# Performance work log

Hardware: AMD Instinct MI355X
Metric: run time of the kernel (lower is better)

Reference implementation:

```python
import jax, jax.numpy as jnp
import numpy as np

DIM = 2048
HID = 2730  # dim*mlp_ratio // (1 + top_k)
E = 8
K = 2
B, T = 4, 2048


def setup_inputs() -> dict:
    key = jax.random.key(0)
    ks = jax.random.split(key, 8)
    s = 0.02
    return {
        "x": jax.random.normal(ks[0], (B, T, DIM), jnp.float32),
        "router_w": jax.random.normal(ks[1], (DIM, E), jnp.float32) * s,
        "sw1": jax.random.normal(ks[2], (DIM, HID), jnp.float32) * s,
        "sw2": jax.random.normal(ks[3], (HID, DIM), jnp.float32) * s,
        "sw3": jax.random.normal(ks[4], (DIM, HID), jnp.float32) * s,
        "ew1": jax.random.normal(ks[5], (E, DIM, HID), jnp.float32) * s,
        "ew2": jax.random.normal(ks[6], (E, HID, DIM), jnp.float32) * s,
        "ew3": jax.random.normal(ks[7], (E, DIM, HID), jnp.float32) * s,
    }


def _expert(x, w1, w2, w3):
    return (jax.nn.silu(x @ w1) * (x @ w3)) @ w2


def reference(x, router_w, sw1, sw2, sw3, ew1, ew2, ew3):
    # eval-mode forward (no router noise, no aux loss)
    out = _expert(x, sw1, sw2, sw3)  # shared expert, [B,T,C]
    logits = x @ router_w            # [B,T,E]
    probs = jax.nn.softmax(logits, axis=-1)
    topv, topi = jax.lax.top_k(probs, K)           # [B,T,K]
    topv = topv / topv.sum(-1, keepdims=True)      # renormalize
    # dense combine weights [B,T,E]: w[...,e] = sum_k topv_k * (topi_k == e)
    onehot = jax.nn.one_hot(topi, E, dtype=x.dtype)  # [B,T,K,E]
    w = jnp.einsum("btk,btke->bte", topv, onehot)
    for e in range(E):  # fixed small loop over experts
        out = out + w[..., e:e + 1] * _expert(x, ew1[e], ew2[e], ew3[e])
    return out
```

## Files before the change

### kernel.cpp

```cpp
#include <hip/hip_runtime.h>
#include <hip/hip_bf16.h>
#include <stdio.h>

#define DIM 2048
#define HID 2730
#define HID_PAD 2816
#define NE 8
#define NTOK 8192
#define NROWS 24576
#define BM 128
#define BN 128
#define BK 64
#define LDK 72

typedef __bf16 v8bf __attribute__((ext_vector_type(8)));
typedef float v4f  __attribute__((ext_vector_type(4)));


__global__ void moe_zero_f4(float4* __restrict__ p, int n4){
  int i = blockIdx.x*blockDim.x + threadIdx.x;
  if (i < n4) p[i] = make_float4(0.f,0.f,0.f,0.f);
}

__global__ void moe_zero_i(int* __restrict__ p, int n){
  int i = threadIdx.x;
  if (i < n) p[i] = 0;
}

__global__ void moe_cast_x(const float* __restrict__ x, __hip_bfloat16* __restrict__ xb){
  int i = (blockIdx.x*blockDim.x + threadIdx.x)*4;
  float4 v = *reinterpret_cast<const float4*>(x + i);
  __hip_bfloat16 o[4];
  o[0]=__float2bfloat16(v.x); o[1]=__float2bfloat16(v.y);
  o[2]=__float2bfloat16(v.z); o[3]=__float2bfloat16(v.w);
  unsigned long long u; __builtin_memcpy(&u, o, 8);
  *reinterpret_cast<unsigned long long*>(xb + i) = u;
}

__global__ void moe_tcast(const float* __restrict__ srcE, const float* __restrict__ srcS,
                          __hip_bfloat16* __restrict__ dst, int R, int C, int Cp, int Rp){
  int e = blockIdx.z;
  const float* src = (e < NE) ? (srcE + (size_t)e*R*C) : srcS;
  __hip_bfloat16* d = dst + (size_t)e*Cp*Rp;
  __shared__ float tile[32][33];
  int c0 = blockIdx.x*32, r0 = blockIdx.y*32;
  #pragma unroll
  for (int i=0;i<4;i++){
    int r = r0 + threadIdx.y + i*8, c = c0 + threadIdx.x;
    float v = (r < R && c < C) ? src[(size_t)r*C + c] : 0.0f;
    tile[threadIdx.y + i*8][threadIdx.x] = v;
  }
  __syncthreads();
  #pragma unroll
  for (int i=0;i<4;i++){
    int c = c0 + threadIdx.y + i*8, r = r0 + threadIdx.x;
    if (c < Cp && r < Rp)
      d[(size_t)c*Rp + r] = __float2bfloat16(tile[threadIdx.x][threadIdx.y + i*8]);
  }
}


__global__ __launch_bounds__(256) void moe_router(
    const float* __restrict__ x, const float* __restrict__ rw,
    float* __restrict__ topw, int* __restrict__ cnt, int* __restrict__ bucket){
  int wav = threadIdx.x >> 6, lane = threadIdx.x & 63;
  int t = blockIdx.x*4 + wav;
  const float* xr = x + (size_t)t*DIM;
  float a[NE];
  #pragma unroll
  for (int e=0;e<NE;e++) a[e]=0.f;
  for (int d0 = lane; d0 < DIM; d0 += 64){
    float xv = xr[d0];
    const float* rr = rw + d0*NE;
    #pragma unroll
    for (int e=0;e<NE;e++) a[e] += xv * rr[e];
  }
  #pragma unroll
  for (int e=0;e<NE;e++){
    float v = a[e];
    #pragma unroll
    for (int o=32;o>0;o>>=1) v += __shfl_xor(v, o);
    a[e]=v;
  }
  if (lane == 0){
    float m = a[0];
    for (int e=1;e<NE;e++) m = fmaxf(m, a[e]);
    float p[NE];
    for (int e=0;e<NE;e++) p[e] = expf(a[e]-m);
    int e0=0;
    for (int e=1;e<NE;e++) if (p[e] > p[e0]) e0=e;
    int e1 = (e0==0)?1:0;
    for (int e=0;e<NE;e++) if (e!=e0 && p[e] > p[e1]) e1=e;
    float ss = p[e0]+p[e1];
    topw[t*2]   = p[e0]/ss;
    topw[t*2+1] = p[e1]/ss;
    int p0 = atomicAdd(&cnt[e0],1); bucket[e0*16384 + p0] = t*2;
    int p1 = atomicAdd(&cnt[e1],1); bucket[e1*16384 + p1] = t*2+1;
  }
}

__global__ void moe_prefix(const int* __restrict__ cnt, int* __restrict__ base){
  if (threadIdx.x==0 && blockIdx.x==0){
    int b=0; base[0]=0;
    for (int e=0;e<NE;e++){ b += cnt[e]; base[e+1]=b; }
    base[9] = base[8] + NTOK;
  }
}

__global__ void moe_fill(const int* __restrict__ cnt, const int* __restrict__ base,
                         const int* __restrict__ bucket, const float* __restrict__ topw,
                         int* __restrict__ row_token, float* __restrict__ row_weight){
  int idx = blockIdx.x*blockDim.x + threadIdx.x;
  if (idx < NE*16384){
    int e = idx >> 14, p = idx & 16383;
    if (p < cnt[e]){
      int slot = bucket[idx];
      int row = base[e] + p;
      row_token[row]  = slot >> 1;
      row_weight[row] = topw[slot];
    }
  } else {
    int t = idx - NE*16384;
    row_token[16384 + t]  = t;
    row_weight[16384 + t] = 1.0f;
  }
}


__global__ __launch_bounds__(256, 2) void moe_gemm1(
    const __hip_bfloat16* __restrict__ xb,
    const __hip_bfloat16* __restrict__ w1t,
    const __hip_bfloat16* __restrict__ w3t,
    const int* __restrict__ row_token,
    const int* __restrict__ base_,
    __hip_bfloat16* __restrict__ g)
{
  int e   = blockIdx.z;
  int base = base_[e];
  int cnt  = base_[e+1] - base;
  int m0  = blockIdx.y * BM;
  if (m0 >= cnt) return;
  int n0  = blockIdx.x * BN;

  __shared__ __align__(16) unsigned short lA [BM][LDK];
  __shared__ __align__(16) unsigned short lB1[BN][LDK];
  __shared__ __align__(16) unsigned short lB3[BN][LDK];
  __shared__ int tok[BM];

  int tid = threadIdx.x;
  if (tid < BM){
    int r = m0 + tid;
    tok[tid] = row_token[base + (r < cnt ? r : m0)];
  }
  __syncthreads();

  const __hip_bfloat16* w1e = w1t + (size_t)e*HID_PAD*DIM;
  const __hip_bfloat16* w3e = w3t + (size_t)e*HID_PAD*DIM;

  const __hip_bfloat16* aSrc[4]; const __hip_bfloat16* b1Src[4]; const __hip_bfloat16* b3Src[4];
  unsigned short* aDst[4]; unsigned short* b1Dst[4]; unsigned short* b3Dst[4];
  #pragma unroll
  for (int i=0;i<4;i++){
    int c = tid + i*256;
    int row = c >> 3, col = (c & 7)*8;
    aSrc[i]  = xb  + (size_t)tok[row]*DIM + col;
    b1Src[i] = w1e + (size_t)(n0+row)*DIM + col;
    b3Src[i] = w3e + (size_t)(n0+row)*DIM + col;
    aDst[i]  = &lA [row][col];
    b1Dst[i] = &lB1[row][col];
    b3Dst[i] = &lB3[row][col];
  }

  int wav = tid >> 6, lane = tid & 63;
  int wm = (wav & 1)*64, wn = (wav >> 1)*64;
  int lm = lane & 15, lq = lane >> 4;

  v4f acc1[4][4], acc3[4][4];
  v4f vz = {0.f,0.f,0.f,0.f};
  #pragma unroll
  for (int i=0;i<4;i++)
    #pragma unroll
    for (int j=0;j<4;j++){ acc1[i][j]=vz; acc3[i][j]=vz; }

  for (int k0 = 0; k0 < DIM; k0 += BK){
    #pragma unroll
    for (int i=0;i<4;i++){
      *reinterpret_cast<uint4*>(aDst[i])  = *reinterpret_cast<const uint4*>(aSrc[i]  + k0);
      *reinterpret_cast<uint4*>(b1Dst[i]) = *reinterpret_cast<const uint4*>(b1Src[i] + k0);
      *reinterpret_cast<uint4*>(b3Dst[i]) = *reinterpret_cast<const uint4*>(b3Src[i] + k0);
    }
    __syncthreads();
    #pragma unroll
    for (int ks=0; ks<2; ks++){
      v8bf af[4], b1f[4], b3f[4];
      #pragma unroll
      for (int i=0;i<4;i++){
        af[i]  = *reinterpret_cast<const v8bf*>(&lA [wm + i*16 + lm][ks*32 + lq*8]);
        b1f[i] = *reinterpret_cast<const v8bf*>(&lB1[wn + i*16 + lm][ks*32 + lq*8]);
        b3f[i] = *reinterpret_cast<const v8bf*>(&lB3[wn + i*16 + lm][ks*32 + lq*8]);
      }
      #pragma unroll
      for (int i=0;i<4;i++)
        #pragma unroll
        for (int j=0;j<4;j++){
          acc1[i][j] = __builtin_amdgcn_mfma_f32_16x16x32_bf16(af[i], b1f[j], acc1[i][j], 0,0,0);
          acc3[i][j] = __builtin_amdgcn_mfma_f32_16x16x32_bf16(af[i], b3f[j], acc3[i][j], 0,0,0);
        }
    }
    __syncthreads();
  }

  #pragma unroll
  for (int i=0;i<4;i++){
    #pragma unroll
    for (int r=0;r<4;r++){
      int ml = wm + i*16 + lq*4 + r;
      if (m0 + ml < cnt){
        size_t grow = (size_t)(base + m0 + ml) * HID_PAD;
        #pragma unroll
        for (int j=0;j<4;j++){
          float s1 = acc1[i][j][r];
          float s3 = acc3[i][j][r];
          float gv = (s1 / (1.0f + __expf(-s1))) * s3;
          g[grow + n0 + wn + j*16 + lm] = __float2bfloat16(gv);
        }
      }
    }
  }
}


__global__ __launch_bounds__(256, 2) void moe_gemm2(
    const __hip_bfloat16* __restrict__ g,
    const __hip_bfloat16* __restrict__ w2t,
    const int* __restrict__ row_token,
    const float* __restrict__ row_weight,
    const int* __restrict__ base_,
    float* __restrict__ out)
{
  int e = blockIdx.z;
  int base = base_[e];
  int cnt  = base_[e+1] - base;
  int m0 = blockIdx.y * BM;
  if (m0 >= cnt) return;
  int n0 = blockIdx.x * BN;

  __shared__ __align__(16) unsigned short lA[BM][LDK];
  __shared__ __align__(16) unsigned short lB[BN][LDK];
  __shared__ int   tok[BM];
  __shared__ float wgt[BM];

  int tid = threadIdx.x;
  if (tid < BM){
    int r = m0 + tid;
    bool v = (r < cnt);
    tok[tid] = v ? row_token[base + r]  : 0;
    wgt[tid] = v ? row_weight[base + r] : 0.0f;
  }
  __syncthreads();

  const __hip_bfloat16* w2e = w2t + (size_t)e*DIM*HID_PAD;

  const __hip_bfloat16* aSrc[4]; const __hip_bfloat16* bSrc[4];
  unsigned short* aDst[4]; unsigned short* bDst[4];
  #pragma unroll
  for (int i=0;i<4;i++){
    int c = tid + i*256;
    int row = c >> 3, col = (c & 7)*8;
    aSrc[i] = g   + (size_t)(base + m0 + row)*HID_PAD + col;
    bSrc[i] = w2e + (size_t)(n0 + row)*HID_PAD + col;
    aDst[i] = &lA[row][col];
    bDst[i] = &lB[row][col];
  }

  int wav = tid >> 6, lane = tid & 63;
  int wm = (wav & 1)*64, wn = (wav >> 1)*64;
  int lm = lane & 15, lq = lane >> 4;

  v4f acc[4][4];
  v4f vz = {0.f,0.f,0.f,0.f};
  #pragma unroll
  for (int i=0;i<4;i++)
    #pragma unroll
    for (int j=0;j<4;j++) acc[i][j]=vz;

  for (int k0 = 0; k0 < HID_PAD; k0 += BK){
    #pragma unroll
    for (int i=0;i<4;i++){
      *reinterpret_cast<uint4*>(aDst[i]) = *reinterpret_cast<const uint4*>(aSrc[i] + k0);
      *reinterpret_cast<uint4*>(bDst[i]) = *reinterpret_cast<const uint4*>(bSrc[i] + k0);
    }
    __syncthreads();
    #pragma unroll
    for (int ks=0; ks<2; ks++){
      v8bf af[4], bf[4];
      #pragma unroll
      for (int i=0;i<4;i++){
        af[i] = *reinterpret_cast<const v8bf*>(&lA[wm + i*16 + lm][ks*32 + lq*8]);
        bf[i] = *reinterpret_cast<const v8bf*>(&lB[wn + i*16 + lm][ks*32 + lq*8]);
      }
      #pragma unroll
      for (int i=0;i<4;i++)
        #pragma unroll
        for (int j=0;j<4;j++)
          acc[i][j] = __builtin_amdgcn_mfma_f32_16x16x32_bf16(af[i], bf[j], acc[i][j], 0,0,0);
    }
    __syncthreads();
  }

  #pragma unroll
  for (int i=0;i<4;i++){
    #pragma unroll
    for (int r=0;r<4;r++){
      int ml = wm + i*16 + lq*4 + r;
      if (m0 + ml < cnt){
        int   t  = tok[ml];
        float wv = wgt[ml];
        #pragma unroll
        for (int j=0;j<4;j++){
          atomicAdd(out + (size_t)t*DIM + n0 + wn + j*16 + lm, wv * acc[i][j][r]);
        }
      }
    }
  }
}


extern "C" void kernel_launch(void* const* d_in, const int* in_sizes, int n_in,
                              void* d_out, int out_size, void* d_ws, size_t ws_size,
                              hipStream_t stream) {
  const float* x   = (const float*)d_in[0];
  const float* rw  = (const float*)d_in[1];
  const float* sw1 = (const float*)d_in[2];
  const float* sw2 = (const float*)d_in[3];
  const float* sw3 = (const float*)d_in[4];
  const float* ew1 = (const float*)d_in[5];
  const float* ew2 = (const float*)d_in[6];
  const float* ew3 = (const float*)d_in[7];
  float* out = (float*)d_out;

  char* ws = (char*)d_ws;
  size_t off = 0;
  auto nxt = [&](size_t b) -> char* {
    char* p = ws + off; off += (b + 255) & ~(size_t)255; return p;
  };
  __hip_bfloat16* xb  = (__hip_bfloat16*)nxt((size_t)NTOK*DIM*2);
  __hip_bfloat16* w1t = (__hip_bfloat16*)nxt((size_t)9*HID_PAD*DIM*2);
  __hip_bfloat16* w3t = (__hip_bfloat16*)nxt((size_t)9*HID_PAD*DIM*2);
  __hip_bfloat16* w2t = (__hip_bfloat16*)nxt((size_t)9*DIM*HID_PAD*2);
  __hip_bfloat16* g   = (__hip_bfloat16*)nxt((size_t)NROWS*HID_PAD*2);
  float* topw      = (float*)nxt(16384*4);
  int*   cnt       = (int*)  nxt(32);
  int*   base_     = (int*)  nxt(64);
  int*   bucket    = (int*)  nxt(NE*16384*4);
  int*   row_token = (int*)  nxt(NROWS*4);
  float* row_weight= (float*)nxt(NROWS*4);

  if (off > ws_size) {
    fprintf(stderr, "MoE kernel: ws too small (%zu needed, %zu given)\n", off, ws_size);
    return;
  }

  moe_zero_f4<<<16384, 256, 0, stream>>>((float4*)out, NTOK*DIM/4);
  moe_zero_i<<<1, 32, 0, stream>>>(cnt, NE);
  moe_cast_x<<<16384, 256, 0, stream>>>(x, xb);

  dim3 tb(32,8);
  moe_tcast<<<dim3(88,64,9), tb, 0, stream>>>(ew1, sw1, w1t, DIM, HID, HID_PAD, DIM);
  moe_tcast<<<dim3(88,64,9), tb, 0, stream>>>(ew3, sw3, w3t, DIM, HID, HID_PAD, DIM);
  moe_tcast<<<dim3(64,88,9), tb, 0, stream>>>(ew2, sw2, w2t, HID, DIM, DIM, HID_PAD);

  moe_router<<<NTOK/4, 256, 0, stream>>>(x, rw, topw, cnt, bucket);
  moe_prefix<<<1, 1, 0, stream>>>(cnt, base_);
  moe_fill<<<544, 256, 0, stream>>>(cnt, base_, bucket, topw, row_token, row_weight);

  moe_gemm1<<<dim3(22,128,9), 256, 0, stream>>>(xb, w1t, w3t, row_token, base_, g);
  moe_gemm2<<<dim3(16,128,9), 256, 0, stream>>>(g, w2t, row_token, row_weight, base_, out);
}
```

Baseline: 2.000 ms.

## Use direct global-to-LDS loads with XOR swizzle and replace atomic scatter with combine

Both grouped GEMMs now stage tiles with global_load_lds, writing straight from global memory into LDS, and use an unpadded XOR-swizzled layout in place of the padded one to avoid bank conflicts. The second GEMM now writes weighted per-row results into a buffer that aliases the w1t/w3t workspace, instead of doing float atomicAdd into the output. A new combine kernel then sums the shared-expert row and the two routed rows per token through an inverse map built in moe_fill. The output zeroing kernel is dropped, and gemm2 occupancy is raised to 3 blocks per SM. The risks are the extra pass over a large fp32 intermediate and the aliasing, which is only safe because gemm1 has finished before gemm2 overwrites its weights.

```diff
diff --git a/kernel.cpp b/kernel.cpp
--- a/kernel.cpp
+++ b/kernel.cpp
@@ -11,16 +11,15 @@
 #define BM 128
 #define BN 128
 #define BK 64
-#define LDK 72
 
 typedef __bf16 v8bf __attribute__((ext_vector_type(8)));
 typedef float v4f  __attribute__((ext_vector_type(4)));
 
-
-__global__ void moe_zero_f4(float4* __restrict__ p, int n4){
-  int i = blockIdx.x*blockDim.x + threadIdx.x;
-  if (i < n4) p[i] = make_float4(0.f,0.f,0.f,0.f);
-}
+__device__ __forceinline__ void gload16(const void* g, void* l){
+  __builtin_amdgcn_global_load_lds((const __attribute__((address_space(1))) void*)g,
+                                   (__attribute__((address_space(3))) void*)l, 16, 0, 0);
+}
+
 
 __global__ void moe_zero_i(int* __restrict__ p, int n){
   int i = threadIdx.x;
@@ -109,7 +108,8 @@
 
 __global__ void moe_fill(const int* __restrict__ cnt, const int* __restrict__ base,
                          const int* __restrict__ bucket, const float* __restrict__ topw,
-                         int* __restrict__ row_token, float* __restrict__ row_weight){
+                         int* __restrict__ row_token, float* __restrict__ row_weight,
+                         int* __restrict__ inv){
   int idx = blockIdx.x*blockDim.x + threadIdx.x;
   if (idx < NE*16384){
     int e = idx >> 14, p = idx & 16383;
@@ -118,6 +118,7 @@
       int row = base[e] + p;
       row_token[row]  = slot >> 1;
       row_weight[row] = topw[slot];
+      inv[slot] = row;
     }
   } else {
     int t = idx - NE*16384;
@@ -142,9 +143,9 @@
   if (m0 >= cnt) return;
   int n0  = blockIdx.x * BN;
 
-  __shared__ __align__(16) unsigned short lA [BM][LDK];
-  __shared__ __align__(16) unsigned short lB1[BN][LDK];
-  __shared__ __align__(16) unsigned short lB3[BN][LDK];
+  __shared__ __align__(16) unsigned short lA [BM][BK];
+  __shared__ __align__(16) unsigned short lB1[BN][BK];
+  __shared__ __align__(16) unsigned short lB3[BN][BK];
   __shared__ int tok[BM];
 
   int tid = threadIdx.x;
@@ -157,23 +158,26 @@
   const __hip_bfloat16* w1e = w1t + (size_t)e*HID_PAD*DIM;
   const __hip_bfloat16* w3e = w3t + (size_t)e*HID_PAD*DIM;
 
-  const __hip_bfloat16* aSrc[4]; const __hip_bfloat16* b1Src[4]; const __hip_bfloat16* b3Src[4];
-  unsigned short* aDst[4]; unsigned short* b1Dst[4]; unsigned short* b3Dst[4];
-  #pragma unroll
-  for (int i=0;i<4;i++){
-    int c = tid + i*256;
-    int row = c >> 3, col = (c & 7)*8;
-    aSrc[i]  = xb  + (size_t)tok[row]*DIM + col;
-    b1Src[i] = w1e + (size_t)(n0+row)*DIM + col;
-    b3Src[i] = w3e + (size_t)(n0+row)*DIM + col;
-    aDst[i]  = &lA [row][col];
-    b1Dst[i] = &lB1[row][col];
-    b3Dst[i] = &lB3[row][col];
-  }
-
   int wav = tid >> 6, lane = tid & 63;
+
+  const __hip_bfloat16 *aS[4], *b1S[4], *b3S[4];
+  unsigned short *aL[4], *b1L[4], *b3L[4];
+  #pragma unroll
+  for (int i=0;i<4;i++){
+    int c = wav*256 + i*64 + lane;
+    int r = c >> 3, p = c & 7, q = p ^ (r & 7);
+    aS[i]  = xb  + (size_t)tok[r]*DIM + q*8;
+    b1S[i] = w1e + (size_t)(n0+r)*DIM + q*8;
+    b3S[i] = w3e + (size_t)(n0+r)*DIM + q*8;
+    int c0 = wav*256 + i*64;
+    aL[i]  = &lA [0][0] + c0*8;
+    b1L[i] = &lB1[0][0] + c0*8;
+    b3L[i] = &lB3[0][0] + c0*8;
+  }
+
   int wm = (wav & 1)*64, wn = (wav >> 1)*64;
   int lm = lane & 15, lq = lane >> 4;
+  int sw = lm & 7;
 
   v4f acc1[4][4], acc3[4][4];
   v4f vz = {0.f,0.f,0.f,0.f};
@@ -185,9 +189,9 @@
   for (int k0 = 0; k0 < DIM; k0 += BK){
     #pragma unroll
     for (int i=0;i<4;i++){
-      *reinterpret_cast<uint4*>(aDst[i])  = *reinterpret_cast<const uint4*>(aSrc[i]  + k0);
-      *reinterpret_cast<uint4*>(b1Dst[i]) = *reinterpret_cast<const uint4*>(b1Src[i] + k0);
-      *reinterpret_cast<uint4*>(b3Dst[i]) = *reinterpret_cast<const uint4*>(b3Src[i] + k0);
+      gload16(aS[i]  + k0, aL[i]);
+      gload16(b1S[i] + k0, b1L[i]);
+      gload16(b3S[i] + k0, b3L[i]);
     }
     __syncthreads();
     #pragma unroll
@@ -195,9 +199,10 @@
       v8bf af[4], b1f[4], b3f[4];
       #pragma unroll
       for (int i=0;i<4;i++){
-        af[i]  = *reinterpret_cast<const v8bf*>(&lA [wm + i*16 + lm][ks*32 + lq*8]);
-        b1f[i] = *reinterpret_cast<const v8bf*>(&lB1[wn + i*16 + lm][ks*32 + lq*8]);
-        b3f[i] = *reinterpret_cast<const v8bf*>(&lB3[wn + i*16 + lm][ks*32 + lq*8]);
+        int qa = ((ks*4 + lq) ^ sw)*8;
+        af[i]  = *reinterpret_cast<const v8bf*>(&lA [wm + i*16 + lm][qa]);
+        b1f[i] = *reinterpret_cast<const v8bf*>(&lB1[wn + i*16 + lm][qa]);
+        b3f[i] = *reinterpret_cast<const v8bf*>(&lB3[wn + i*16 + lm][qa]);
       }
       #pragma unroll
       for (int i=0;i<4;i++)
@@ -230,13 +235,12 @@
 }
 
 
-__global__ __launch_bounds__(256, 2) void moe_gemm2(
+__global__ __launch_bounds__(256, 3) void moe_gemm2(
     const __hip_bfloat16* __restrict__ g,
     const __hip_bfloat16* __restrict__ w2t,
-    const int* __restrict__ row_token,
     const float* __restrict__ row_weight,
     const int* __restrict__ base_,
-    float* __restrict__ out)
+    float* __restrict__ y)
 {
   int e = blockIdx.z;
   int base = base_[e];
@@ -245,37 +249,37 @@
   if (m0 >= cnt) return;
   int n0 = blockIdx.x * BN;
 
-  __shared__ __align__(16) unsigned short lA[BM][LDK];
-  __shared__ __align__(16) unsigned short lB[BN][LDK];
-  __shared__ int   tok[BM];
+  __shared__ __align__(16) unsigned short lA[BM][BK];
+  __shared__ __align__(16) unsigned short lB[BN][BK];
   __shared__ float wgt[BM];
 
   int tid = threadIdx.x;
   if (tid < BM){
     int r = m0 + tid;
-    bool v = (r < cnt);
-    tok[tid] = v ? row_token[base + r]  : 0;
-    wgt[tid] = v ? row_weight[base + r] : 0.0f;
+    wgt[tid] = (r < cnt) ? row_weight[base + r] : 0.0f;
   }
   __syncthreads();
 
   const __hip_bfloat16* w2e = w2t + (size_t)e*DIM*HID_PAD;
 
-  const __hip_bfloat16* aSrc[4]; const __hip_bfloat16* bSrc[4];
-  unsigned short* aDst[4]; unsigned short* bDst[4];
-  #pragma unroll
-  for (int i=0;i<4;i++){
-    int c = tid + i*256;
-    int row = c >> 3, col = (c & 7)*8;
-    aSrc[i] = g   + (size_t)(base + m0 + row)*HID_PAD + col;
-    bSrc[i] = w2e + (size_t)(n0 + row)*HID_PAD + col;
-    aDst[i] = &lA[row][col];
-    bDst[i] = &lB[row][col];
-  }
-
   int wav = tid >> 6, lane = tid & 63;
+
+  const __hip_bfloat16 *aS[4], *bS[4];
+  unsigned short *aL[4], *bL[4];
+  #pragma unroll
+  for (int i=0;i<4;i++){
+    int c = wav*256 + i*64 + lane;
+    int r = c >> 3, p = c & 7, q = p ^ (r & 7);
+    aS[i] = g   + (size_t)(base + m0 + r)*HID_PAD + q*8;
+    bS[i] = w2e + (size_t)(n0 + r)*HID_PAD + q*8;
+    int c0 = wav*256 + i*64;
+    aL[i] = &lA[0][0] + c0*8;
+    bL[i] = &lB[0][0] + c0*8;
+  }
+
   int wm = (wav & 1)*64, wn = (wav >> 1)*64;
   int lm = lane & 15, lq = lane >> 4;
+  int sw = lm & 7;
 
   v4f acc[4][4];
   v4f vz = {0.f,0.f,0.f,0.f};
@@ -287,8 +291,8 @@
   for (int k0 = 0; k0 < HID_PAD; k0 += BK){
     #pragma unroll
     for (int i=0;i<4;i++){
-      *reinterpret_cast<uint4*>(aDst[i]) = *reinterpret_cast<const uint4*>(aSrc[i] + k0);
-      *reinterpret_cast<uint4*>(bDst[i]) = *reinterpret_cast<const uint4*>(bSrc[i] + k0);
+      gload16(aS[i] + k0, aL[i]);
+      gload16(bS[i] + k0, bL[i]);
     }
     __syncthreads();
     #pragma unroll
@@ -296,8 +300,9 @@
       v8bf af[4], bf[4];
       #pragma unroll
       for (int i=0;i<4;i++){
-        af[i] = *reinterpret_cast<const v8bf*>(&lA[wm + i*16 + lm][ks*32 + lq*8]);
-        bf[i] = *reinterpret_cast<const v8bf*>(&lB[wn + i*16 + lm][ks*32 + lq*8]);
+        int qa = ((ks*4 + lq) ^ sw)*8;
+        af[i] = *reinterpret_cast<const v8bf*>(&lA[wm + i*16 + lm][qa]);
+        bf[i] = *reinterpret_cast<const v8bf*>(&lB[wn + i*16 + lm][qa]);
       }
       #pragma unroll
       for (int i=0;i<4;i++)
@@ -314,15 +319,27 @@
     for (int r=0;r<4;r++){
       int ml = wm + i*16 + lq*4 + r;
       if (m0 + ml < cnt){
-        int   t  = tok[ml];
         float wv = wgt[ml];
+        size_t yrow = (size_t)(base + m0 + ml) * DIM;
         #pragma unroll
-        for (int j=0;j<4;j++){
-          atomicAdd(out + (size_t)t*DIM + n0 + wn + j*16 + lm, wv * acc[i][j][r]);
-        }
+        for (int j=0;j<4;j++)
+          y[yrow + n0 + wn + j*16 + lm] = wv * acc[i][j][r];
       }
     }
   }
+}
+
+
+__global__ __launch_bounds__(256) void moe_combine(
+    const float4* __restrict__ y, const int* __restrict__ inv, float4* __restrict__ out){
+  int idx = blockIdx.x*blockDim.x + threadIdx.x;
+  int t = idx >> 9, d = idx & 511;
+  float4 s = y[(((size_t)16384 + t) << 9) + d];
+  int r0 = inv[t*2], r1 = inv[t*2+1];
+  float4 a = y[((size_t)r0 << 9) + d];
+  float4 b = y[((size_t)r1 << 9) + d];
+  s.x += a.x + b.x; s.y += a.y + b.y; s.z += a.z + b.z; s.w += a.w + b.w;
+  out[idx] = s;
 }
 
 
@@ -355,13 +372,16 @@
   int*   bucket    = (int*)  nxt(NE*16384*4);
   int*   row_token = (int*)  nxt(NROWS*4);
   float* row_weight= (float*)nxt(NROWS*4);
+  int*   inv       = (int*)  nxt(16384*4);
+
+  static_assert((size_t)NROWS*DIM*4 <= 2*((size_t)9*HID_PAD*DIM*2), "y alias overflow");
+  float* y = (float*)w1t;
 
   if (off > ws_size) {
     fprintf(stderr, "MoE kernel: ws too small (%zu needed, %zu given)\n", off, ws_size);
     return;
   }
 
-  moe_zero_f4<<<16384, 256, 0, stream>>>((float4*)out, NTOK*DIM/4);
   moe_zero_i<<<1, 32, 0, stream>>>(cnt, NE);
   moe_cast_x<<<16384, 256, 0, stream>>>(x, xb);
 
@@ -372,8 +392,9 @@
 
   moe_router<<<NTOK/4, 256, 0, stream>>>(x, rw, topw, cnt, bucket);
   moe_prefix<<<1, 1, 0, stream>>>(cnt, base_);
-  moe_fill<<<544, 256, 0, stream>>>(cnt, base_, bucket, topw, row_token, row_weight);
+  moe_fill<<<544, 256, 0, stream>>>(cnt, base_, bucket, topw, row_token, row_weight, inv);
 
   moe_gemm1<<<dim3(22,128,9), 256, 0, stream>>>(xb, w1t, w3t, row_token, base_, g);
-  moe_gemm2<<<dim3(16,128,9), 256, 0, stream>>>(g, w2t, row_token, row_weight, base_, out);
-}
+  moe_gemm2<<<dim3(16,128,9), 256, 0, stream>>>(g, w2t, row_weight, base_, y);
+  moe_combine<<<16384, 256, 0, stream>>>((const float4*)y, inv, (float4*)out);
+}
```

Result: faster. 1.864 ms (-6.8%).
